# Kernel tuning notes

Hardware: AMD Instinct MI355X
Metric: run time of the kernel (lower is better)

The kernel has to match this reference:

```python
import jax, jax.numpy as jnp
import numpy as np

EMB = 1024
HEADS = 8
INNER = EMB // HEADS          # 128
HEAD_DIM = INNER // HEADS     # 16
SCALE = INNER ** -0.5         # note: module scales by inner_dim, not head_dim
EPS = 1e-5


def setup_inputs() -> dict:
    key = jax.random.key(0)
    ks = jax.random.split(key, 4)
    b, n = 16, 1024
    x = jax.random.normal(ks[0], (b, n, EMB), dtype=jnp.float32)
    gamma = jnp.ones((EMB,), dtype=jnp.float32)
    beta = jnp.zeros((EMB,), dtype=jnp.float32)
    w_qkv = jax.random.normal(ks[1], (EMB, 3 * INNER), dtype=jnp.float32) * (EMB ** -0.5)
    w_proj = jax.random.normal(ks[2], (INNER, EMB), dtype=jnp.float32) * (INNER ** -0.5)
    b_proj = jnp.zeros((EMB,), dtype=jnp.float32)
    return {"x": x, "gamma": gamma, "beta": beta, "w_qkv": w_qkv,
            "w_proj": w_proj, "b_proj": b_proj}


def reference(x, gamma, beta, w_qkv, w_proj, b_proj):
    b, n, _ = x.shape
    # LayerNorm
    mu = jnp.mean(x, axis=-1, keepdims=True)
    var = jnp.var(x, axis=-1, keepdims=True)
    xn = (x - mu) * jax.lax.rsqrt(var + EPS) * gamma + beta
    # QKV projection (bias=False): [b, n, 3*INNER]
    qkv = jnp.einsum('bne,ef->bnf', xn, w_qkv)
    q, k, v = jnp.split(qkv, 3, axis=-1)
    to_heads = lambda a: a.reshape(b, n, HEADS, HEAD_DIM).transpose(0, 2, 1, 3)
    q, k, v = to_heads(q) * SCALE, to_heads(k), to_heads(v)
    # full score matrix [b, h, n, n] (as the original einsum does)
    attn = jax.nn.softmax(jnp.einsum('bhid,bhjd->bhij', q, k), axis=-1)
    out = jnp.einsum('bhij,bhjd->bhid', attn, v)
    out = out.transpose(0, 2, 1, 3).reshape(b, n, INNER)
    return jnp.einsum('bni,ie->bne', out, w_proj) + b_proj
```

## Files before the change

kernel.cpp:

```cpp
#include <hip/hip_runtime.h>

#define LOG2E 1.44269504088896340736f
#define QSCALE (0.08838834764831845f * LOG2E)

using short8 = __attribute__((ext_vector_type(8))) short;
using f32x4  = __attribute__((ext_vector_type(4))) float;
using f32x16 = __attribute__((ext_vector_type(16))) float;

union U16B { uint4 u; short8 s; };

typedef __attribute__((address_space(3))) unsigned char lds_byte;
typedef const __attribute__((address_space(1))) unsigned char glb_byte;
#define GLOAD16(gp, lp) __builtin_amdgcn_global_load_lds((glb_byte*)(gp), (lds_byte*)(lp), 16, 0, 0)

static __device__ __forceinline__ unsigned short f2bf(float f){
  union { float f; unsigned int i; } c; c.f = f;
  unsigned int i = c.i;
  i += 0x7fffu + ((i >> 16) & 1u);
  return (unsigned short)(i >> 16);
}

__global__ __launch_bounds__(256) void k_ln(const float* __restrict__ x,
                                            const float* __restrict__ gamma,
                                            const float* __restrict__ beta,
                                            unsigned short* __restrict__ xn,
                                            const float* __restrict__ wqkv,
                                            const float* __restrict__ wproj,
                                            unsigned short* __restrict__ wqkvT,
                                            unsigned short* __restrict__ wprojT){
  if (blockIdx.x < 4096){
    const int tok = (blockIdx.x*256 + threadIdx.x) >> 6;
    const int l = threadIdx.x & 63;
    const float4* xr = (const float4*)(x + (size_t)tok*1024);
    float4 v[4];
    #pragma unroll
    for (int i=0;i<4;i++) v[i] = xr[l + i*64];
    float s = 0.f, s2 = 0.f;
    #pragma unroll
    for (int i=0;i<4;i++){
      s  += v[i].x+v[i].y+v[i].z+v[i].w;
      s2 += v[i].x*v[i].x+v[i].y*v[i].y+v[i].z*v[i].z+v[i].w*v[i].w;
    }
    #pragma unroll
    for (int o=32;o;o>>=1){ s += __shfl_xor(s,o); s2 += __shfl_xor(s2,o); }
    float mu   = s*(1.0f/1024.0f);
    float rstd = rsqrtf(s2*(1.0f/1024.0f) - mu*mu + 1e-5f);
    ushort4* xo = (ushort4*)(xn + (size_t)tok*1024);
    #pragma unroll
    for (int i=0;i<4;i++){
      float4 g = ((const float4*)gamma)[l + i*64];
      float4 b = ((const float4*)beta)[l + i*64];
      ushort4 o;
      o.x = f2bf((v[i].x-mu)*rstd*g.x + b.x);
      o.y = f2bf((v[i].y-mu)*rstd*g.y + b.y);
      o.z = f2bf((v[i].z-mu)*rstd*g.z + b.z);
      o.w = f2bf((v[i].w-mu)*rstd*g.w + b.w);
      xo[l + i*64] = o;
    }
  } else {
    int t = (blockIdx.x - 4096)*256 + threadIdx.x;
    if (t < 49152){
      int n = t>>7, k0 = (t&127)*8;
      float sc = (n < 128) ? QSCALE : 1.0f;
      const float* src = wqkv + (size_t)k0*384 + n;
      ushort4 lo, hi;
      lo.x = f2bf(src[0]*sc);    lo.y = f2bf(src[384]*sc);
      lo.z = f2bf(src[768]*sc);  lo.w = f2bf(src[1152]*sc);
      hi.x = f2bf(src[1536]*sc); hi.y = f2bf(src[1920]*sc);
      hi.z = f2bf(src[2304]*sc); hi.w = f2bf(src[2688]*sc);
      *(ushort4*)(wqkvT + (size_t)n*1024 + k0)     = lo;
      *(ushort4*)(wqkvT + (size_t)n*1024 + k0 + 4) = hi;
    } else {
      int t2 = t - 49152;
      int n = t2>>4, k0 = (t2&15)*8;
      const float* src = wproj + (size_t)k0*1024 + n;
      ushort4 lo, hi;
      lo.x = f2bf(src[0]);    lo.y = f2bf(src[1024]);
      lo.z = f2bf(src[2048]); lo.w = f2bf(src[3072]);
      hi.x = f2bf(src[4096]); hi.y = f2bf(src[5120]);
      hi.z = f2bf(src[6144]); hi.w = f2bf(src[7168]);
      *(ushort4*)(wprojT + (size_t)n*128 + k0)     = lo;
      *(ushort4*)(wprojT + (size_t)n*128 + k0 + 4) = hi;
    }
  }
}

__global__ __launch_bounds__(256) void k_qkv(const unsigned short* __restrict__ xn,
                                             const unsigned short* __restrict__ wT,
                                             unsigned short* __restrict__ q,
                                             unsigned short* __restrict__ kbuf,
                                             unsigned short* __restrict__ vT){
  __shared__ __align__(16) unsigned short sm[2][64*64 + 128*64];
  const int tid = threadIdx.x;
  const int w = tid>>6, l = tid&63;
  const int m0 = blockIdx.x*64;
  const int sec = blockIdx.y;
  const int nb = sec*128;
  const int wm = (w>>1)*32, wn = (w&1)*64;
  f32x4 acc[2][4] = {};

  auto stage = [&](int buf, int k0){
    unsigned short* sA = &sm[buf][0];
    unsigned short* sB = &sm[buf][4096];
    #pragma unroll
    for (int i=0;i<2;i++){
      int chunk = i*256 + tid;
      int row = chunk>>3;
      int ch = (tid&7) ^ (row&7);
      GLOAD16(xn + (size_t)(m0+row)*1024 + k0 + ch*8,
              (char*)sA + (i*256 + w*64)*16);
    }
    #pragma unroll
    for (int i=0;i<4;i++){
      int chunk = i*256 + tid;
      int row = chunk>>3;
      int ch = (tid&7) ^ (row&7);
      GLOAD16(wT + (size_t)(nb+row)*1024 + k0 + ch*8,
              (char*)sB + (i*256 + w*64)*16);
    }
  };

  stage(0, 0);
  for (int t=0; t<16; ++t){
    const int cur = t & 1;
    if (t < 15){
      stage(cur^1, (t+1)<<6);
      asm volatile("s_waitcnt vmcnt(6)" ::: "memory");
    } else {
      asm volatile("s_waitcnt vmcnt(0)" ::: "memory");
    }
    __builtin_amdgcn_s_barrier();
    const unsigned short* sA = &sm[cur][0];
    const unsigned short* sB = &sm[cur][4096];
    #pragma unroll
    for (int s=0; s<2; ++s){
      short8 af[2], bfr[4];
      #pragma unroll
      for (int i=0;i<2;i++){
        int row = wm + i*16 + (l&15);
        U16B ta; ta.u = *(const uint4*)((const char*)sA + row*128 + ((s*64 + (l>>4)*16) ^ ((row&7)<<4)));
        af[i] = ta.s;
      }
      #pragma unroll
      for (int j=0;j<4;j++){
        int col = wn + j*16 + (l&15);
        U16B tb; tb.u = *(const uint4*)((const char*)sB + col*128 + ((s*64 + (l>>4)*16) ^ ((col&7)<<4)));
        bfr[j] = tb.s;
      }
      #pragma unroll
      for (int i=0;i<2;i++)
        #pragma unroll
        for (int j=0;j<4;j++)
          acc[i][j] = __builtin_amdgcn_mfma_f32_16x16x32_bf16(af[i], bfr[j], acc[i][j], 0,0,0);
    }
    __builtin_amdgcn_s_barrier();
  }

  const int b  = m0 >> 10;
  const int n0 = m0 & 1023;
  unsigned short* ep = &sm[0][0];
  if (sec < 2){
    #pragma unroll
    for (int fm=0; fm<2; ++fm)
      #pragma unroll
      for (int fn=0; fn<4; ++fn){
        int colf = wn + fn*16 + (l&15);
        #pragma unroll
        for (int i=0;i<4;i++){
          int row = wm + fm*16 + (l>>4)*4 + i;
          *(unsigned short*)((char*)ep + row*256 + ((2*colf) ^ ((row&15)<<4))) = f2bf(acc[fm][fn][i]);
        }
      }
    __syncthreads();
    unsigned short* dst = (sec==0) ? q : kbuf;
    #pragma unroll
    for (int it=0; it<4; ++it){
      int chunk = it*256 + tid;
      int tokl = chunk>>4, cc = chunk&15;
      uint4 vv = *(const uint4*)((const char*)ep + tokl*256 + ((cc*16) ^ ((tokl&15)<<4)));
      int h = cc>>1, d0 = (cc&1)*8;
      *(uint4*)(dst + ((size_t)(b*8 + h)*1024 + n0 + tokl)*16 + d0) = vv;
    }
  } else {
    #pragma unroll
    for (int fm=0; fm<2; ++fm)
      #pragma unroll
      for (int fn=0; fn<4; ++fn){
        int colf = wn + fn*16 + (l&15);
        int r0 = wm + fm*16 + (l>>4)*4;
        ushort4 pk;
        pk.x = f2bf(acc[fm][fn][0]); pk.y = f2bf(acc[fm][fn][1]);
        pk.z = f2bf(acc[fm][fn][2]); pk.w = f2bf(acc[fm][fn][3]);
        *(ushort4*)((char*)ep + colf*128 + ((2*r0) ^ ((colf&7)<<4))) = pk;
      }
    __syncthreads();
    #pragma unroll
    for (int it=0; it<4; ++it){
      int chunk = it*256 + tid;
      int f = chunk>>3, cc = chunk&7;
      uint4 vv = *(const uint4*)((const char*)ep + f*128 + ((cc*16) ^ ((f&7)<<4)));
      int h = f>>4, d = f&15;
      unsigned short* dp = vT + ((size_t)(b*8 + h)*16 + d)*1024 + n0 + (cc>>1)*16 + (cc&1)*4;
      *(uint2*)dp       = make_uint2(vv.x, vv.y);
      *(uint2*)(dp + 8) = make_uint2(vv.z, vv.w);
    }
  }
}

__global__ __launch_bounds__(256) void k_attn(const unsigned short* __restrict__ q,
                                              const unsigned short* __restrict__ kbuf,
                                              const unsigned short* __restrict__ vT,
                                              unsigned short* __restrict__ aout){
  const int bh = blockIdx.x;
  const int qc = blockIdx.y;
  const int w = threadIdx.x>>6, l = threadIdx.x&63;
  const int l31 = l&31, hi = l>>5;
  const int h = bh & 7;
  const int qrow = qc*128 + w*32 + l31;
  U16B qf_u; qf_u.u = *(const uint4*)(q + ((size_t)bh*1024 + qrow)*16 + hi*8);
  const short8 qf = qf_u.s;
  const unsigned short* kptr = kbuf + (size_t)bh*1024*16 + (size_t)l31*16 + hi*8;
  const unsigned short* vptr = vT + (size_t)bh*16*1024 + (size_t)(l31 & 15)*1024 + hi*8;
  const bool vok = (l31 < 16);
  const unsigned int ob = ((l31==16)||(l31==20)) ? 0x3F803F80u : 0u;
  const uint4 cvu = make_uint4(ob, ob, ob, ob);
  f32x16 acc = {};
  const f32x16 zz = {};

  U16B kf; kf.u = *(const uint4*)kptr; kptr += 512;
  U16B kn; kn.u = *(const uint4*)kptr; kptr += 512;
  U16B v0, v1; v0.u = cvu; v1.u = cvu;
  if (vok){ v0.u = *(const uint4*)vptr; v1.u = *(const uint4*)(vptr + 16); }
  vptr += 32;
  f32x16 sv = __builtin_amdgcn_mfma_f32_32x32x16_bf16(kf.s, qf, zz, 0,0,0);

  for (int t=0; t<32; ++t){
    U16B knn; knn.u = *(const uint4*)kptr; kptr += 512;
    U16B v0n, v1n; v0n.u = cvu; v1n.u = cvu;
    if (vok){ v0n.u = *(const uint4*)vptr; v1n.u = *(const uint4*)(vptr + 16); }
    vptr += 32;
    f32x16 svn = __builtin_amdgcn_mfma_f32_32x32x16_bf16(kn.s, qf, zz, 0,0,0);
    unsigned int u[8];
    #pragma unroll
    for (int j=0;j<8;j++){
      float a = __builtin_amdgcn_exp2f(sv[2*j]);
      float b = __builtin_amdgcn_exp2f(sv[2*j+1]);
      asm("v_cvt_pk_bf16_f32 %0, %1, %2" : "=v"(u[j]) : "v"(a), "v"(b));
    }
    U16B p0, p1;
    p0.u.x = u[0]; p0.u.y = u[1]; p0.u.z = u[2]; p0.u.w = u[3];
    p1.u.x = u[4]; p1.u.y = u[5]; p1.u.z = u[6]; p1.u.w = u[7];
    __builtin_amdgcn_s_setprio(1);
    acc = __builtin_amdgcn_mfma_f32_32x32x16_bf16(v0.s, p0.s, acc, 0,0,0);
    acc = __builtin_amdgcn_mfma_f32_32x32x16_bf16(v1.s, p1.s, acc, 0,0,0);
    __builtin_amdgcn_s_setprio(0);
    sv = svn; kn = knn; v0 = v0n; v1 = v1n;
  }
  float inv = 1.0f/acc[8];
  const size_t tok = (size_t)(bh>>3)*1024 + qrow;
  ushort4 o;
  o.x = f2bf(acc[0]*inv); o.y = f2bf(acc[1]*inv); o.z = f2bf(acc[2]*inv); o.w = f2bf(acc[3]*inv);
  *(ushort4*)(aout + tok*128 + h*16 + hi*4) = o;
  o.x = f2bf(acc[4]*inv); o.y = f2bf(acc[5]*inv); o.z = f2bf(acc[6]*inv); o.w = f2bf(acc[7]*inv);
  *(ushort4*)(aout + tok*128 + h*16 + 8 + hi*4) = o;
}

__global__ __launch_bounds__(256) void k_proj(const unsigned short* __restrict__ aout,
                                              const unsigned short* __restrict__ wT,
                                              const float* __restrict__ bias,
                                              float* __restrict__ out){
  __shared__ __align__(16) unsigned short sA[128*128];
  __shared__ __align__(16) unsigned short sB[128*128];
  const int tid = threadIdx.x;
  const int w = tid>>6, l = tid&63;
  const int m0 = blockIdx.x*128, nb = blockIdx.y*128;
  #pragma unroll
  for (int i=0;i<8;i++){
    int chunk = i*256 + tid;
    int row = chunk>>4;
    int ch = (tid&15) ^ (row&15);
    GLOAD16(aout + (size_t)(m0+row)*128 + ch*8, (char*)sA + (i*256 + w*64)*16);
  }
  #pragma unroll
  for (int i=0;i<8;i++){
    int chunk = i*256 + tid;
    int row = chunk>>4;
    int ch = (tid&15) ^ (row&15);
    GLOAD16(wT + (size_t)(nb+row)*128 + ch*8, (char*)sB + (i*256 + w*64)*16);
  }
  __syncthreads();
  const int wm = (w>>1)*64, wn = (w&1)*64;
  f32x4 acc[4][4] = {};
  #pragma unroll
  for (int s=0; s<4; ++s){
    short8 af[4], bfr[4];
    #pragma unroll
    for (int i=0;i<4;i++){
      int row = wm + i*16 + (l&15);
      U16B ta; ta.u = *(const uint4*)((const char*)sA + row*256 + ((s*64 + (l>>4)*16) ^ ((row&15)<<4)));
      af[i] = ta.s;
      int col = wn + i*16 + (l&15);
      U16B tb; tb.u = *(const uint4*)((const char*)sB + col*256 + ((s*64 + (l>>4)*16) ^ ((col&15)<<4)));
      bfr[i] = tb.s;
    }
    #pragma unroll
    for (int i=0;i<4;i++)
      #pragma unroll
      for (int j=0;j<4;j++)
        acc[i][j] = __builtin_amdgcn_mfma_f32_16x16x32_bf16(af[i], bfr[j], acc[i][j], 0,0,0);
  }
  #pragma unroll
  for (int fn=0; fn<4; ++fn){
    int col = nb + wn + fn*16 + (l&15);
    float bv = bias[col];
    #pragma unroll
    for (int fm=0; fm<4; ++fm)
      #pragma unroll
      for (int i=0;i<4;i++)
        out[(size_t)(m0 + wm + fm*16 + (l>>4)*4 + i)*1024 + col] = acc[fm][fn][i] + bv;
  }
}

extern "C" void kernel_launch(void* const* d_in, const int* in_sizes, int n_in,
                              void* d_out, int out_size, void* d_ws, size_t ws_size,
                              hipStream_t stream){
  (void)in_sizes; (void)n_in; (void)out_size; (void)ws_size;
  const float* x     = (const float*)d_in[0];
  const float* gamma = (const float*)d_in[1];
  const float* beta  = (const float*)d_in[2];
  const float* wqkv  = (const float*)d_in[3];
  const float* wproj = (const float*)d_in[4];
  const float* bias  = (const float*)d_in[5];
  float* out = (float*)d_out;
  char* ws = (char*)d_ws;
  unsigned short* xn = (unsigned short*)ws;
  unsigned short* q  = (unsigned short*)(ws + 33554432);
  unsigned short* kb = (unsigned short*)(ws + 33554432 + 4194304);
  unsigned short* vT = (unsigned short*)(ws + 33554432 + 2*4194304);
  unsigned short* ao = (unsigned short*)(ws + 33554432 + 3*4194304);
  unsigned short* wqkvT = (unsigned short*)(ws + 33554432 + 4*4194304);
  unsigned short* wprojT = (unsigned short*)(ws + 33554432 + 4*4194304 + 786432);
  k_ln  <<<dim3(4352), dim3(256), 0, stream>>>(x, gamma, beta, xn, wqkv, wproj, wqkvT, wprojT);
  k_qkv <<<dim3(256,3), dim3(256), 0, stream>>>(xn, wqkvT, q, kb, vT);
  k_attn<<<dim3(128,8), dim3(256), 0, stream>>>(q, kb, vT, ao);
  k_proj<<<dim3(128,8), dim3(256), 0, stream>>>(ao, wprojT, bias, out);
}
```

Measured before the change: 89.88 us.

## Enlarge QKV GEMM tile to 128x128 and drop LDS double buffering

The QKV projection kernel now computes a 128-token by 128-column tile per block, with each wave holding a 64x64 accumulator instead of 32x64. This raises data reuse per LDS load and halves the grid from 768 to 384 blocks. The two-stage LDS pipeline with explicit vmcnt waits is replaced by a single buffer with syncthreads around each k-step, so global loads no longer overlap MFMA work. The epilogues are widened to match the larger tile. The smaller grid and the loss of load/compute overlap may hurt occupancy and latency hiding.

New measurement: 96.28 us. 7.1% more time.

```diff
diff --git a/kernel.cpp b/kernel.cpp
--- a/kernel.cpp
+++ b/kernel.cpp
@@ -90,20 +90,19 @@
                                              unsigned short* __restrict__ q,
                                              unsigned short* __restrict__ kbuf,
                                              unsigned short* __restrict__ vT){
-  __shared__ __align__(16) unsigned short sm[2][64*64 + 128*64];
+  __shared__ __align__(16) unsigned short sm[2*128*64];
+  unsigned short* sA = sm;
+  unsigned short* sB = sm + 8192;
   const int tid = threadIdx.x;
   const int w = tid>>6, l = tid&63;
-  const int m0 = blockIdx.x*64;
+  const int m0 = blockIdx.x*128;
   const int sec = blockIdx.y;
   const int nb = sec*128;
-  const int wm = (w>>1)*32, wn = (w&1)*64;
-  f32x4 acc[2][4] = {};
-
-  auto stage = [&](int buf, int k0){
-    unsigned short* sA = &sm[buf][0];
-    unsigned short* sB = &sm[buf][4096];
-    #pragma unroll
-    for (int i=0;i<2;i++){
+  const int wm = (w>>1)*64, wn = (w&1)*64;
+  f32x4 acc[4][4] = {};
+  for (int k0=0; k0<1024; k0+=64){
+    #pragma unroll
+    for (int i=0;i<4;i++){
       int chunk = i*256 + tid;
       int row = chunk>>3;
       int ch = (tid&7) ^ (row&7);
@@ -118,50 +117,34 @@
       GLOAD16(wT + (size_t)(nb+row)*1024 + k0 + ch*8,
               (char*)sB + (i*256 + w*64)*16);
     }
-  };
-
-  stage(0, 0);
-  for (int t=0; t<16; ++t){
-    const int cur = t & 1;
-    if (t < 15){
-      stage(cur^1, (t+1)<<6);
-      asm volatile("s_waitcnt vmcnt(6)" ::: "memory");
-    } else {
-      asm volatile("s_waitcnt vmcnt(0)" ::: "memory");
-    }
-    __builtin_amdgcn_s_barrier();
-    const unsigned short* sA = &sm[cur][0];
-    const unsigned short* sB = &sm[cur][4096];
+    __syncthreads();
     #pragma unroll
     for (int s=0; s<2; ++s){
-      short8 af[2], bfr[4];
-      #pragma unroll
-      for (int i=0;i<2;i++){
+      short8 af[4], bfr[4];
+      #pragma unroll
+      for (int i=0;i<4;i++){
         int row = wm + i*16 + (l&15);
         U16B ta; ta.u = *(const uint4*)((const char*)sA + row*128 + ((s*64 + (l>>4)*16) ^ ((row&7)<<4)));
         af[i] = ta.s;
+        int col = wn + i*16 + (l&15);
+        U16B tb; tb.u = *(const uint4*)((const char*)sB + col*128 + ((s*64 + (l>>4)*16) ^ ((col&7)<<4)));
+        bfr[i] = tb.s;
       }
       #pragma unroll
-      for (int j=0;j<4;j++){
-        int col = wn + j*16 + (l&15);
-        U16B tb; tb.u = *(const uint4*)((const char*)sB + col*128 + ((s*64 + (l>>4)*16) ^ ((col&7)<<4)));
-        bfr[j] = tb.s;
-      }
-      #pragma unroll
-      for (int i=0;i<2;i++)
+      for (int i=0;i<4;i++)
         #pragma unroll
         for (int j=0;j<4;j++)
           acc[i][j] = __builtin_amdgcn_mfma_f32_16x16x32_bf16(af[i], bfr[j], acc[i][j], 0,0,0);
     }
-    __builtin_amdgcn_s_barrier();
+    __syncthreads();
   }
 
   const int b  = m0 >> 10;
   const int n0 = m0 & 1023;
-  unsigned short* ep = &sm[0][0];
+  unsigned short* ep = sm;
   if (sec < 2){
     #pragma unroll
-    for (int fm=0; fm<2; ++fm)
+    for (int fm=0; fm<4; ++fm)
       #pragma unroll
       for (int fn=0; fn<4; ++fn){
         int colf = wn + fn*16 + (l&15);
@@ -174,7 +157,7 @@
     __syncthreads();
     unsigned short* dst = (sec==0) ? q : kbuf;
     #pragma unroll
-    for (int it=0; it<4; ++it){
+    for (int it=0; it<8; ++it){
       int chunk = it*256 + tid;
       int tokl = chunk>>4, cc = chunk&15;
       uint4 vv = *(const uint4*)((const char*)ep + tokl*256 + ((cc*16) ^ ((tokl&15)<<4)));
@@ -183,7 +166,7 @@
     }
   } else {
     #pragma unroll
-    for (int fm=0; fm<2; ++fm)
+    for (int fm=0; fm<4; ++fm)
       #pragma unroll
       for (int fn=0; fn<4; ++fn){
         int colf = wn + fn*16 + (l&15);
@@ -191,14 +174,14 @@
         ushort4 pk;
         pk.x = f2bf(acc[fm][fn][0]); pk.y = f2bf(acc[fm][fn][1]);
         pk.z = f2bf(acc[fm][fn][2]); pk.w = f2bf(acc[fm][fn][3]);
-        *(ushort4*)((char*)ep + colf*128 + ((2*r0) ^ ((colf&7)<<4))) = pk;
+        *(ushort4*)((char*)ep + colf*256 + ((2*r0) ^ ((colf&15)<<4))) = pk;
       }
     __syncthreads();
     #pragma unroll
-    for (int it=0; it<4; ++it){
+    for (int it=0; it<8; ++it){
       int chunk = it*256 + tid;
-      int f = chunk>>3, cc = chunk&7;
-      uint4 vv = *(const uint4*)((const char*)ep + f*128 + ((cc*16) ^ ((f&7)<<4)));
+      int f = chunk>>4, cc = chunk&15;
+      uint4 vv = *(const uint4*)((const char*)ep + f*256 + ((cc*16) ^ ((f&15)<<4)));
       int h = f>>4, d = f&15;
       unsigned short* dp = vT + ((size_t)(b*8 + h)*16 + d)*1024 + n0 + (cc>>1)*16 + (cc&1)*4;
       *(uint2*)dp       = make_uint2(vv.x, vv.y);
@@ -341,7 +324,7 @@
   unsigned short* wqkvT = (unsigned short*)(ws + 33554432 + 4*4194304);
   unsigned short* wprojT = (unsigned short*)(ws + 33554432 + 4*4194304 + 786432);
   k_ln  <<<dim3(4352), dim3(256), 0, stream>>>(x, gamma, beta, xn, wqkv, wproj, wqkvT, wprojT);
-  k_qkv <<<dim3(256,3), dim3(256), 0, stream>>>(xn, wqkvT, q, kb, vT);
+  k_qkv <<<dim3(128,3), dim3(256), 0, stream>>>(xn, wqkvT, q, kb, vT);
   k_attn<<<dim3(128,8), dim3(256), 0, stream>>>(q, kb, vT, ao);
   k_proj<<<dim3(128,8), dim3(256), 0, stream>>>(ao, wprojT, bias, out);
 }
```

## Process two query tiles per wave in attention to reuse K/V loads

Applied to the files above, without the earlier changes.

Each wave in the attention kernel now handles two 32-row query tiles (rows offset by 128) that share each loaded K and V fragment, and the grid's query dimension is halved to match. The S-MFMA is no longer software-pipelined one step ahead; V prefetch goes two iterations deep instead. This halves global K/V traffic per query and gives more independent MFMA/exp work per iteration to hide latency. In exchange it doubles accumulator registers, which may lower occupancy, and launches half as many blocks.

After: 93.27 us. 1.04x slower.

```diff
diff --git a/kernel.cpp b/kernel.cpp
--- a/kernel.cpp
+++ b/kernel.cpp
@@ -216,15 +216,18 @@
   const int w = threadIdx.x>>6, l = threadIdx.x&63;
   const int l31 = l&31, hi = l>>5;
   const int h = bh & 7;
-  const int qrow = qc*128 + w*32 + l31;
-  U16B qf_u; qf_u.u = *(const uint4*)(q + ((size_t)bh*1024 + qrow)*16 + hi*8);
-  const short8 qf = qf_u.s;
-  const unsigned short* kptr = kbuf + (size_t)bh*1024*16 + (size_t)l31*16 + hi*8;
-  const unsigned short* vptr = vT + (size_t)bh*16*1024 + (size_t)(l31 & 15)*1024 + hi*8;
+  const int qrowA = qc*256 + w*32 + l31;
+  const int qrowB = qrowA + 128;
+  U16B qa_u; qa_u.u = *(const uint4*)(q + ((size_t)bh*1024 + qrowA)*16 + hi*8);
+  U16B qb_u; qb_u.u = *(const uint4*)(q + ((size_t)bh*1024 + qrowB)*16 + hi*8);
+  const short8 qfA = qa_u.s;
+  const short8 qfB = qb_u.s;
+  const unsigned short* kptr = kbuf + (size_t)bh*16384 + (size_t)l31*16 + hi*8;
+  const unsigned short* vptr = vT + (size_t)bh*16384 + (size_t)(l31 & 15)*1024 + hi*8;
   const bool vok = (l31 < 16);
   const unsigned int ob = ((l31==16)||(l31==20)) ? 0x3F803F80u : 0u;
   const uint4 cvu = make_uint4(ob, ob, ob, ob);
-  f32x16 acc = {};
+  f32x16 accA = {}, accB = {};
   const f32x16 zz = {};
 
   U16B kf; kf.u = *(const uint4*)kptr; kptr += 512;
@@ -232,37 +235,60 @@
   U16B v0, v1; v0.u = cvu; v1.u = cvu;
   if (vok){ v0.u = *(const uint4*)vptr; v1.u = *(const uint4*)(vptr + 16); }
   vptr += 32;
-  f32x16 sv = __builtin_amdgcn_mfma_f32_32x32x16_bf16(kf.s, qf, zz, 0,0,0);
+  U16B v0n, v1n; v0n.u = cvu; v1n.u = cvu;
+  if (vok){ v0n.u = *(const uint4*)vptr; v1n.u = *(const uint4*)(vptr + 16); }
+  vptr += 32;
 
   for (int t=0; t<32; ++t){
     U16B knn; knn.u = *(const uint4*)kptr; kptr += 512;
-    U16B v0n, v1n; v0n.u = cvu; v1n.u = cvu;
-    if (vok){ v0n.u = *(const uint4*)vptr; v1n.u = *(const uint4*)(vptr + 16); }
+    U16B v0nn, v1nn; v0nn.u = cvu; v1nn.u = cvu;
+    if (vok){ v0nn.u = *(const uint4*)vptr; v1nn.u = *(const uint4*)(vptr + 16); }
     vptr += 32;
-    f32x16 svn = __builtin_amdgcn_mfma_f32_32x32x16_bf16(kn.s, qf, zz, 0,0,0);
+    f32x16 svA = __builtin_amdgcn_mfma_f32_32x32x16_bf16(kf.s, qfA, zz, 0,0,0);
+    f32x16 svB = __builtin_amdgcn_mfma_f32_32x32x16_bf16(kf.s, qfB, zz, 0,0,0);
     unsigned int u[8];
     #pragma unroll
     for (int j=0;j<8;j++){
-      float a = __builtin_amdgcn_exp2f(sv[2*j]);
-      float b = __builtin_amdgcn_exp2f(sv[2*j+1]);
+      float a = __builtin_amdgcn_exp2f(svA[2*j]);
+      float b = __builtin_amdgcn_exp2f(svA[2*j+1]);
       asm("v_cvt_pk_bf16_f32 %0, %1, %2" : "=v"(u[j]) : "v"(a), "v"(b));
     }
     U16B p0, p1;
     p0.u.x = u[0]; p0.u.y = u[1]; p0.u.z = u[2]; p0.u.w = u[3];
     p1.u.x = u[4]; p1.u.y = u[5]; p1.u.z = u[6]; p1.u.w = u[7];
     __builtin_amdgcn_s_setprio(1);
-    acc = __builtin_amdgcn_mfma_f32_32x32x16_bf16(v0.s, p0.s, acc, 0,0,0);
-    acc = __builtin_amdgcn_mfma_f32_32x32x16_bf16(v1.s, p1.s, acc, 0,0,0);
+    accA = __builtin_amdgcn_mfma_f32_32x32x16_bf16(v0.s, p0.s, accA, 0,0,0);
+    accA = __builtin_amdgcn_mfma_f32_32x32x16_bf16(v1.s, p1.s, accA, 0,0,0);
     __builtin_amdgcn_s_setprio(0);
-    sv = svn; kn = knn; v0 = v0n; v1 = v1n;
-  }
-  float inv = 1.0f/acc[8];
-  const size_t tok = (size_t)(bh>>3)*1024 + qrow;
+    #pragma unroll
+    for (int j=0;j<8;j++){
+      float a = __builtin_amdgcn_exp2f(svB[2*j]);
+      float b = __builtin_amdgcn_exp2f(svB[2*j+1]);
+      asm("v_cvt_pk_bf16_f32 %0, %1, %2" : "=v"(u[j]) : "v"(a), "v"(b));
+    }
+    U16B r0, r1;
+    r0.u.x = u[0]; r0.u.y = u[1]; r0.u.z = u[2]; r0.u.w = u[3];
+    r1.u.x = u[4]; r1.u.y = u[5]; r1.u.z = u[6]; r1.u.w = u[7];
+    __builtin_amdgcn_s_setprio(1);
+    accB = __builtin_amdgcn_mfma_f32_32x32x16_bf16(v0.s, r0.s, accB, 0,0,0);
+    accB = __builtin_amdgcn_mfma_f32_32x32x16_bf16(v1.s, r1.s, accB, 0,0,0);
+    __builtin_amdgcn_s_setprio(0);
+    kf = kn; kn = knn;
+    v0 = v0n; v1 = v1n; v0n = v0nn; v1n = v1nn;
+  }
+  const size_t tokA = (size_t)(bh>>3)*1024 + qrowA;
+  const size_t tokB = (size_t)(bh>>3)*1024 + qrowB;
+  float invA = 1.0f/accA[8];
   ushort4 o;
-  o.x = f2bf(acc[0]*inv); o.y = f2bf(acc[1]*inv); o.z = f2bf(acc[2]*inv); o.w = f2bf(acc[3]*inv);
-  *(ushort4*)(aout + tok*128 + h*16 + hi*4) = o;
-  o.x = f2bf(acc[4]*inv); o.y = f2bf(acc[5]*inv); o.z = f2bf(acc[6]*inv); o.w = f2bf(acc[7]*inv);
-  *(ushort4*)(aout + tok*128 + h*16 + 8 + hi*4) = o;
+  o.x = f2bf(accA[0]*invA); o.y = f2bf(accA[1]*invA); o.z = f2bf(accA[2]*invA); o.w = f2bf(accA[3]*invA);
+  *(ushort4*)(aout + tokA*128 + h*16 + hi*4) = o;
+  o.x = f2bf(accA[4]*invA); o.y = f2bf(accA[5]*invA); o.z = f2bf(accA[6]*invA); o.w = f2bf(accA[7]*invA);
+  *(ushort4*)(aout + tokA*128 + h*16 + 8 + hi*4) = o;
+  float invB = 1.0f/accB[8];
+  o.x = f2bf(accB[0]*invB); o.y = f2bf(accB[1]*invB); o.z = f2bf(accB[2]*invB); o.w = f2bf(accB[3]*invB);
+  *(ushort4*)(aout + tokB*128 + h*16 + hi*4) = o;
+  o.x = f2bf(accB[4]*invB); o.y = f2bf(accB[5]*invB); o.z = f2bf(accB[6]*invB); o.w = f2bf(accB[7]*invB);
+  *(ushort4*)(aout + tokB*128 + h*16 + 8 + hi*4) = o;
 }
 
 __global__ __launch_bounds__(256) void k_proj(const unsigned short* __restrict__ aout,
@@ -342,6 +368,6 @@
   unsigned short* wprojT = (unsigned short*)(ws + 33554432 + 4*4194304 + 786432);
   k_ln  <<<dim3(4352), dim3(256), 0, stream>>>(x, gamma, beta, xn, wqkv, wproj, wqkvT, wprojT);
   k_qkv <<<dim3(256,3), dim3(256), 0, stream>>>(xn, wqkvT, q, kb, vT);
-  k_attn<<<dim3(128,8), dim3(256), 0, stream>>>(q, kb, vT, ao);
+  k_attn<<<dim3(128,4), dim3(256), 0, stream>>>(q, kb, vT, ao);
   k_proj<<<dim3(128,8), dim3(256), 0, stream>>>(ao, wprojT, bias, out);
 }
```

## Split attention over key range with fp32 partials and add reduce kernel; remap QKV grid

Applied to the files above, without the earlier changes.

The attention kernel now splits the 1024 keys into two halves across a third grid dimension. Each half writes unnormalized fp32 partial numerators and softmax denominators to a workspace, and a new reduce kernel sums them, normalizes and writes bf16 output. This doubles attention parallelism from 1024 to 2048 blocks, which helps fill the CUs. The cost is about 17 MB of extra fp32 traffic and one more launch. Separately, the QKV GEMM uses a 1D grid remapped so that blocks sharing an XCD (bid&7) work on nearby row tiles and all three sections, aiming for better L2 reuse of the xn tiles.

Measured after the change: 99.86 us. 1.11x slower.

```diff
diff --git a/kernel.cpp b/kernel.cpp
--- a/kernel.cpp
+++ b/kernel.cpp
@@ -12,6 +12,8 @@
 typedef __attribute__((address_space(3))) unsigned char lds_byte;
 typedef const __attribute__((address_space(1))) unsigned char glb_byte;
 #define GLOAD16(gp, lp) __builtin_amdgcn_global_load_lds((glb_byte*)(gp), (lds_byte*)(lp), 16, 0, 0)
+
+#define NROW 131072
 
 static __device__ __forceinline__ unsigned short f2bf(float f){
   union { float f; unsigned int i; } c; c.f = f;
@@ -93,8 +95,11 @@
   __shared__ __align__(16) unsigned short sm[2][64*64 + 128*64];
   const int tid = threadIdx.x;
   const int w = tid>>6, l = tid&63;
-  const int m0 = blockIdx.x*64;
-  const int sec = blockIdx.y;
+  const int bid = blockIdx.x;
+  const int X = bid & 7, j = bid >> 3;
+  const int g = X*32 + (j/3);
+  const int sec = j % 3;
+  const int m0 = g*64;
   const int nb = sec*128;
   const int wm = (w>>1)*32, wn = (w&1)*64;
   f32x4 acc[2][4] = {};
@@ -142,16 +147,16 @@
         af[i] = ta.s;
       }
       #pragma unroll
-      for (int j=0;j<4;j++){
-        int col = wn + j*16 + (l&15);
+      for (int jj=0;jj<4;jj++){
+        int col = wn + jj*16 + (l&15);
         U16B tb; tb.u = *(const uint4*)((const char*)sB + col*128 + ((s*64 + (l>>4)*16) ^ ((col&7)<<4)));
-        bfr[j] = tb.s;
+        bfr[jj] = tb.s;
       }
       #pragma unroll
       for (int i=0;i<2;i++)
         #pragma unroll
-        for (int j=0;j<4;j++)
-          acc[i][j] = __builtin_amdgcn_mfma_f32_16x16x32_bf16(af[i], bfr[j], acc[i][j], 0,0,0);
+        for (int jj=0;jj<4;jj++)
+          acc[i][jj] = __builtin_amdgcn_mfma_f32_16x16x32_bf16(af[i], bfr[jj], acc[i][jj], 0,0,0);
     }
     __builtin_amdgcn_s_barrier();
   }
@@ -210,17 +215,17 @@
 __global__ __launch_bounds__(256) void k_attn(const unsigned short* __restrict__ q,
                                               const unsigned short* __restrict__ kbuf,
                                               const unsigned short* __restrict__ vT,
-                                              unsigned short* __restrict__ aout){
+                                              float* __restrict__ pacc){
   const int bh = blockIdx.x;
   const int qc = blockIdx.y;
+  const int sp = blockIdx.z;
   const int w = threadIdx.x>>6, l = threadIdx.x&63;
   const int l31 = l&31, hi = l>>5;
-  const int h = bh & 7;
   const int qrow = qc*128 + w*32 + l31;
   U16B qf_u; qf_u.u = *(const uint4*)(q + ((size_t)bh*1024 + qrow)*16 + hi*8);
   const short8 qf = qf_u.s;
-  const unsigned short* kptr = kbuf + (size_t)bh*1024*16 + (size_t)l31*16 + hi*8;
-  const unsigned short* vptr = vT + (size_t)bh*16*1024 + (size_t)(l31 & 15)*1024 + hi*8;
+  const unsigned short* kptr = kbuf + (size_t)bh*16384 + sp*8192 + (size_t)l31*16 + hi*8;
+  const unsigned short* vptr = vT + (size_t)bh*16384 + (size_t)(l31 & 15)*1024 + sp*512 + hi*8;
   const bool vok = (l31 < 16);
   const unsigned int ob = ((l31==16)||(l31==20)) ? 0x3F803F80u : 0u;
   const uint4 cvu = make_uint4(ob, ob, ob, ob);
@@ -234,7 +239,7 @@
   vptr += 32;
   f32x16 sv = __builtin_amdgcn_mfma_f32_32x32x16_bf16(kf.s, qf, zz, 0,0,0);
 
-  for (int t=0; t<32; ++t){
+  for (int t=0; t<16; ++t){
     U16B knn; knn.u = *(const uint4*)kptr; kptr += 512;
     U16B v0n, v1n; v0n.u = cvu; v1n.u = cvu;
     if (vok){ v0n.u = *(const uint4*)vptr; v1n.u = *(const uint4*)(vptr + 16); }
@@ -256,13 +261,34 @@
     __builtin_amdgcn_s_setprio(0);
     sv = svn; kn = knn; v0 = v0n; v1 = v1n;
   }
-  float inv = 1.0f/acc[8];
-  const size_t tok = (size_t)(bh>>3)*1024 + qrow;
-  ushort4 o;
-  o.x = f2bf(acc[0]*inv); o.y = f2bf(acc[1]*inv); o.z = f2bf(acc[2]*inv); o.w = f2bf(acc[3]*inv);
-  *(ushort4*)(aout + tok*128 + h*16 + hi*4) = o;
-  o.x = f2bf(acc[4]*inv); o.y = f2bf(acc[5]*inv); o.z = f2bf(acc[6]*inv); o.w = f2bf(acc[7]*inv);
-  *(ushort4*)(aout + tok*128 + h*16 + 8 + hi*4) = o;
+  const int row = bh*1024 + qrow;
+  #pragma unroll
+  for (int j=0;j<8;j++){
+    int c = (j>>2)*8 + hi*4 + (j&3);
+    pacc[(size_t)(c*2 + sp)*NROW + row] = acc[j];
+  }
+  if (hi==0) pacc[(size_t)(16*2 + sp)*NROW + row] = acc[8];
+}
+
+__global__ __launch_bounds__(256) void k_reduce(const float* __restrict__ pacc,
+                                                unsigned short* __restrict__ aout){
+  const int row = blockIdx.x*256 + threadIdx.x;
+  float ssum = pacc[(size_t)(16*2+0)*NROW + row] + pacc[(size_t)(16*2+1)*NROW + row];
+  float inv = 1.0f/ssum;
+  const int bh = row >> 10;
+  const int h = bh & 7;
+  const size_t tok = (size_t)(bh>>3)*1024 + (row & 1023);
+  unsigned short* op = aout + tok*128 + h*16;
+  #pragma unroll
+  for (int g4=0; g4<4; ++g4){
+    ushort4 o;
+    float a0 = pacc[(size_t)((g4*4+0)*2+0)*NROW + row] + pacc[(size_t)((g4*4+0)*2+1)*NROW + row];
+    float a1 = pacc[(size_t)((g4*4+1)*2+0)*NROW + row] + pacc[(size_t)((g4*4+1)*2+1)*NROW + row];
+    float a2 = pacc[(size_t)((g4*4+2)*2+0)*NROW + row] + pacc[(size_t)((g4*4+2)*2+1)*NROW + row];
+    float a3 = pacc[(size_t)((g4*4+3)*2+0)*NROW + row] + pacc[(size_t)((g4*4+3)*2+1)*NROW + row];
+    o.x = f2bf(a0*inv); o.y = f2bf(a1*inv); o.z = f2bf(a2*inv); o.w = f2bf(a3*inv);
+    *(ushort4*)(op + g4*4) = o;
+  }
 }
 
 __global__ __launch_bounds__(256) void k_proj(const unsigned short* __restrict__ aout,
@@ -340,8 +366,10 @@
   unsigned short* ao = (unsigned short*)(ws + 33554432 + 3*4194304);
   unsigned short* wqkvT = (unsigned short*)(ws + 33554432 + 4*4194304);
   unsigned short* wprojT = (unsigned short*)(ws + 33554432 + 4*4194304 + 786432);
-  k_ln  <<<dim3(4352), dim3(256), 0, stream>>>(x, gamma, beta, xn, wqkv, wproj, wqkvT, wprojT);
-  k_qkv <<<dim3(256,3), dim3(256), 0, stream>>>(xn, wqkvT, q, kb, vT);
-  k_attn<<<dim3(128,8), dim3(256), 0, stream>>>(q, kb, vT, ao);
-  k_proj<<<dim3(128,8), dim3(256), 0, stream>>>(ao, wprojT, bias, out);
-}
+  float* pacc = (float*)(ws + 51380224);
+  k_ln    <<<dim3(4352), dim3(256), 0, stream>>>(x, gamma, beta, xn, wqkv, wproj, wqkvT, wprojT);
+  k_qkv   <<<dim3(768), dim3(256), 0, stream>>>(xn, wqkvT, q, kb, vT);
+  k_attn  <<<dim3(128,8,2), dim3(256), 0, stream>>>(q, kb, vT, pacc);
+  k_reduce<<<dim3(512), dim3(256), 0, stream>>>(pacc, ao);
+  k_proj  <<<dim3(128,8), dim3(256), 0, stream>>>(ao, wprojT, bias, out);
+}
```
